# Kernel optimization log

Measured on AMD Instinct MI355X. Metric: run time of the kernel, lower is better.

## Reference

```python
import jax, jax.numpy as jnp
import numpy as np

B, T, D = 4096, 200, 64
H = 32  # hidden units of score MLP
NEG_INF = jnp.float32(-2**32 + 1)


def setup_inputs() -> dict:
    key = jax.random.key(0)
    k1, k2, k3, k4, k5 = jax.random.split(key, 5)
    query = jax.random.normal(k1, (B, 1, D), dtype=jnp.float32)
    keys = jax.random.normal(k2, (B, T, D), dtype=jnp.float32)
    mask = jax.random.randint(k3, (B, T), 0, 2) > 0
    mask = mask.at[:, 0].set(True)  # ensure at least one valid key per row
    # Glorot-normal-ish init for the tiny score MLP
    W1 = jax.random.normal(k4, (3 * D, H), dtype=jnp.float32) * jnp.sqrt(2.0 / (3 * D + H))
    b1 = jnp.zeros((H,), dtype=jnp.float32)
    W2 = jax.random.normal(k5, (H, 1), dtype=jnp.float32) * jnp.sqrt(2.0 / (H + 1))
    b2 = jnp.zeros((1,), dtype=jnp.float32)
    return {"query": query, "keys": keys, "mask": mask,
            "W1": W1, "b1": b1, "W2": W2, "b2": b2}


def reference(query, keys, mask, W1, b1, W2, b2):
    b, t, d = keys.shape
    q = jnp.broadcast_to(query, (b, t, d))            # tile query over seq
    att_in = jnp.concatenate([q, keys, q - keys], axis=-1)   # [B,T,3D]
    h = jax.nn.sigmoid(att_in @ W1 + b1)              # [B,T,H]
    score = (h @ W2 + b2)[..., 0]                     # [B,T]
    score = jnp.where(mask, score, NEG_INF)
    w = jax.nn.softmax(score, axis=-1)                # [B,T]
    out = jnp.einsum('bt,btd->bd', w, keys)           # weighted key sum
    return out[:, None, :]                            # [B,1,D]
```

## Files before the change

### kernel.cpp

```cpp
#include <hip/hip_runtime.h>
#include <hip/hip_bf16.h>


#define B 4096
#define T 200
#define D 64
#define H 32
#define LOG2E 1.44269504088896340736f
#define SOFF 16.0f
#define NTILE 13
#define PITCH 68

typedef __attribute__((ext_vector_type(8))) short short8;
typedef __attribute__((ext_vector_type(4))) float f32x4;


__global__ __launch_bounds__(256) void prep_kernel(
        const float* __restrict__ W1,
        const float* __restrict__ b1,
        const float* __restrict__ query,
        float*       __restrict__ ws)
{
    int blk = blockIdx.x;
    int tid = threadIdx.x;
    if (blk < 512) {
        int n = blk * 256 + tid;
        int b = n >> 5;
        int j = n & 31;
        const float* qb = query + (size_t)b * D;
        float acc = b1[j];
        #pragma unroll 8
        for (int i = 0; i < D; ++i)
            acc = fmaf(qb[i], W1[i * H + j] + W1[(128 + i) * H + j], acc);
        ws[n] = acc;
    } else if (blk < 520) {
        int m = (blk - 512) * 256 + tid;
        int e  = m & 7;
        int l  = (m >> 3) & 63;
        int fs = m >> 9;
        int ntile = fs >> 1, kstep = fs & 1;
        int k = kstep * 32 + (l >> 4) * 8 + e;
        int j = ntile * 16 + (l & 15);
        float v = W1[(64 + k) * H + j] - W1[(128 + k) * H + j];
        __hip_bfloat16 hv = __float2bfloat16(v);
        reinterpret_cast<unsigned short*>(ws + 131072)[m] =
            __builtin_bit_cast(unsigned short, hv);
    } else {
        int z = (blk - 520) * 256 + tid;
        float4 zz = {0.f, 0.f, 0.f, 0.f};
        reinterpret_cast<float4*>(ws + 132096)[z] = zz;
    }
}

__device__ __forceinline__ unsigned short bf16u(float x) {
    __hip_bfloat16 h = __float2bfloat16(x);
    return __builtin_bit_cast(unsigned short, h);
}

__global__ __launch_bounds__(256) void attn_pool_kernel(
        const float* __restrict__ keys,
        const int*   __restrict__ mask,
        const unsigned short* __restrict__ wkf,
        const float* __restrict__ qa_all,
        const float* __restrict__ W2,
        float*       __restrict__ num,
        float*       __restrict__ den)
{
    __shared__ float wkbuf[4][16 * PITCH];

    const int tid  = threadIdx.x;
    const int wv   = tid >> 6;
    const int lane = tid & 63;
    const int quad = lane >> 4;
    const int l15  = lane & 15;

    const int gid  = blockIdx.x * 4 + wv;
    const int b    = (int)(((unsigned)gid * 20165u) >> 18);
    const int tile = gid - b * NTILE;

    const short8* wf = reinterpret_cast<const short8*>(wkf);
    short8 bf0 = wf[0 * 64 + lane];
    short8 bf1 = wf[1 * 64 + lane];
    short8 bf2 = wf[2 * 64 + lane];
    short8 bf3 = wf[3 * 64 + lane];

    const float* qa = qa_all + (size_t)b * H;
    const float qa0 = qa[l15];
    const float qa1 = qa[16 + l15];
    const float w20 = W2[l15];
    const float w21 = W2[16 + l15];

    const int t  = tile * 16 + l15;
    const int tr = (t < T) ? t : (T - 1);

    const float4* krow = reinterpret_cast<const float4*>(keys + (size_t)b * (T * D));
    float4 k0 = krow[tr * 16 + quad * 2 + 0];
    float4 k1 = krow[tr * 16 + quad * 2 + 1];
    float4 k2 = krow[tr * 16 + 8 + quad * 2 + 0];
    float4 k3 = krow[tr * 16 + 8 + quad * 2 + 1];
    const int mval = mask[(size_t)b * T + tr];

    short8 a0, a1;
    a0[0] = (short)bf16u(k0.x); a0[1] = (short)bf16u(k0.y);
    a0[2] = (short)bf16u(k0.z); a0[3] = (short)bf16u(k0.w);
    a0[4] = (short)bf16u(k1.x); a0[5] = (short)bf16u(k1.y);
    a0[6] = (short)bf16u(k1.z); a0[7] = (short)bf16u(k1.w);
    a1[0] = (short)bf16u(k2.x); a1[1] = (short)bf16u(k2.y);
    a1[2] = (short)bf16u(k2.z); a1[3] = (short)bf16u(k2.w);
    a1[4] = (short)bf16u(k3.x); a1[5] = (short)bf16u(k3.y);
    a1[6] = (short)bf16u(k3.z); a1[7] = (short)bf16u(k3.w);

    f32x4 c0 = {0.f, 0.f, 0.f, 0.f};
    f32x4 c1 = {0.f, 0.f, 0.f, 0.f};
    c0 = __builtin_amdgcn_mfma_f32_16x16x32_bf16(a0, bf0, c0, 0, 0, 0);
    c0 = __builtin_amdgcn_mfma_f32_16x16x32_bf16(a1, bf1, c0, 0, 0, 0);
    c1 = __builtin_amdgcn_mfma_f32_16x16x32_bf16(a0, bf2, c1, 0, 0, 0);
    c1 = __builtin_amdgcn_mfma_f32_16x16x32_bf16(a1, bf3, c1, 0, 0, 0);

    float p[4];
    #pragma unroll
    for (int r = 0; r < 4; ++r) {
        float x0 = c0[r] + qa0;
        float x1 = c1[r] + qa1;
        float s0 = __builtin_amdgcn_rcpf(1.0f + exp2f(-x0 * LOG2E));
        float s1 = __builtin_amdgcn_rcpf(1.0f + exp2f(-x1 * LOG2E));
        p[r] = fmaf(s0, w20, s1 * w21);
    }
    #pragma unroll
    for (int r = 0; r < 4; ++r) {
        #pragma unroll
        for (int off = 1; off <= 8; off <<= 1)
            p[r] += __shfl_xor(p[r], off, 64);
    }
    const int addr = (l15 >> 2) << 6;
    int q0 = __builtin_amdgcn_ds_bpermute(addr, __builtin_bit_cast(int, p[0]));
    int q1 = __builtin_amdgcn_ds_bpermute(addr, __builtin_bit_cast(int, p[1]));
    int q2 = __builtin_amdgcn_ds_bpermute(addr, __builtin_bit_cast(int, p[2]));
    int q3 = __builtin_amdgcn_ds_bpermute(addr, __builtin_bit_cast(int, p[3]));
    const int rsel = l15 & 3;
    int s01 = (rsel & 1) ? q1 : q0;
    int s23 = (rsel & 1) ? q3 : q2;
    float st = __builtin_bit_cast(float, (rsel & 2) ? s23 : s01);

    const float w = ((t < T) && (mval != 0)) ? exp2f((st - SOFF) * LOG2E) : 0.0f;

    float* wb = wkbuf[wv];
    float4 wk0 = {w * k0.x, w * k0.y, w * k0.z, w * k0.w};
    float4 wk1 = {w * k1.x, w * k1.y, w * k1.z, w * k1.w};
    float4 wk2 = {w * k2.x, w * k2.y, w * k2.z, w * k2.w};
    float4 wk3 = {w * k3.x, w * k3.y, w * k3.z, w * k3.w};
    *reinterpret_cast<float4*>(&wb[l15 * PITCH + quad * 8 + 0]) = wk0;
    *reinterpret_cast<float4*>(&wb[l15 * PITCH + quad * 8 + 4]) = wk1;
    *reinterpret_cast<float4*>(&wb[l15 * PITCH + 32 + quad * 8 + 0]) = wk2;
    *reinterpret_cast<float4*>(&wb[l15 * PITCH + 32 + quad * 8 + 4]) = wk3;

    float dw = w;
    #pragma unroll
    for (int off = 1; off <= 8; off <<= 1)
        dw += __shfl_xor(dw, off, 64);

    float colsum = 0.0f;
    #pragma unroll
    for (int tt = 0; tt < 16; ++tt)
        colsum += wb[tt * PITCH + lane];

    atomicAdd(&num[(size_t)b * D + lane], colsum);
    if (lane == 0) atomicAdd(&den[b], dw);
}

__global__ __launch_bounds__(256) void finalize_kernel(
        const float* __restrict__ num, const float* __restrict__ den,
        float* __restrict__ out)
{
    int i = blockIdx.x * 256 + threadIdx.x;
    out[i] = num[i] * __builtin_amdgcn_rcpf(den[i >> 6]);
}

extern "C" void kernel_launch(void* const* d_in, const int* in_sizes, int n_in,
                              void* d_out, int out_size, void* d_ws, size_t ws_size,
                              hipStream_t stream) {
    const float* query = (const float*)d_in[0];
    const float* keys  = (const float*)d_in[1];
    const int*   mask  = (const int*)d_in[2];
    const float* W1    = (const float*)d_in[3];
    const float* b1    = (const float*)d_in[4];
    const float* W2    = (const float*)d_in[5];

    float* ws = (float*)d_ws;
    float* qa = ws;
    unsigned short* wkf = (unsigned short*)(ws + 131072);
    float* num = ws + 132096;
    float* den = ws + 132096 + 262144;

    prep_kernel<<<780, 256, 0, stream>>>(W1, b1, query, ws);
    attn_pool_kernel<<<(B * NTILE) / 4, 256, 0, stream>>>(keys, mask, wkf, qa, W2,
                                                          num, den);
    finalize_kernel<<<(B * D) / 256, 256, 0, stream>>>(num, den, (float*)d_out);
}
```

Before: 303.4 us.

## Process a full batch row per wavefront and drop atomics and finalize kernel

Each wavefront now loops over all 13 time tiles of one batch row and keeps the weighted key sums and denominator in registers, prefetching the next tile's keys while computing the current one. This removes the zero-init pass, the LDS staging buffer, the global atomics on num/den and the separate finalize launch, and writes normalized outputs directly. In exchange the grid shrinks from ~13k blocks to 1024 blocks, so there is less parallelism for hiding memory latency, and it adds a 16-register accumulator with cross-lane shuffle reductions.

```diff
diff --git a/kernel.cpp b/kernel.cpp
--- a/kernel.cpp
+++ b/kernel.cpp
@@ -9,7 +9,6 @@
 #define LOG2E 1.44269504088896340736f
 #define SOFF 16.0f
 #define NTILE 13
-#define PITCH 68
 
 typedef __attribute__((ext_vector_type(8))) short short8;
 typedef __attribute__((ext_vector_type(4))) float f32x4;
@@ -33,7 +32,7 @@
         for (int i = 0; i < D; ++i)
             acc = fmaf(qb[i], W1[i * H + j] + W1[(128 + i) * H + j], acc);
         ws[n] = acc;
-    } else if (blk < 520) {
+    } else {
         int m = (blk - 512) * 256 + tid;
         int e  = m & 7;
         int l  = (m >> 3) & 63;
@@ -45,10 +44,6 @@
         __hip_bfloat16 hv = __float2bfloat16(v);
         reinterpret_cast<unsigned short*>(ws + 131072)[m] =
             __builtin_bit_cast(unsigned short, hv);
-    } else {
-        int z = (blk - 520) * 256 + tid;
-        float4 zz = {0.f, 0.f, 0.f, 0.f};
-        reinterpret_cast<float4*>(ws + 132096)[z] = zz;
     }
 }
 
@@ -57,26 +52,21 @@
     return __builtin_bit_cast(unsigned short, h);
 }
 
-__global__ __launch_bounds__(256) void attn_pool_kernel(
+__global__ __launch_bounds__(256, 4) void attn_pool_kernel(
         const float* __restrict__ keys,
         const int*   __restrict__ mask,
         const unsigned short* __restrict__ wkf,
         const float* __restrict__ qa_all,
         const float* __restrict__ W2,
-        float*       __restrict__ num,
-        float*       __restrict__ den)
+        float*       __restrict__ out)
 {
-    __shared__ float wkbuf[4][16 * PITCH];
-
     const int tid  = threadIdx.x;
     const int wv   = tid >> 6;
     const int lane = tid & 63;
     const int quad = lane >> 4;
     const int l15  = lane & 15;
 
-    const int gid  = blockIdx.x * 4 + wv;
-    const int b    = (int)(((unsigned)gid * 20165u) >> 18);
-    const int tile = gid - b * NTILE;
+    const int b = blockIdx.x * 4 + wv;
 
     const short8* wf = reinterpret_cast<const short8*>(wkf);
     short8 bf0 = wf[0 * 64 + lane];
@@ -90,90 +80,115 @@
     const float w20 = W2[l15];
     const float w21 = W2[16 + l15];
 
-    const int t  = tile * 16 + l15;
-    const int tr = (t < T) ? t : (T - 1);
-
     const float4* krow = reinterpret_cast<const float4*>(keys + (size_t)b * (T * D));
-    float4 k0 = krow[tr * 16 + quad * 2 + 0];
-    float4 k1 = krow[tr * 16 + quad * 2 + 1];
-    float4 k2 = krow[tr * 16 + 8 + quad * 2 + 0];
-    float4 k3 = krow[tr * 16 + 8 + quad * 2 + 1];
-    const int mval = mask[(size_t)b * T + tr];
-
-    short8 a0, a1;
-    a0[0] = (short)bf16u(k0.x); a0[1] = (short)bf16u(k0.y);
-    a0[2] = (short)bf16u(k0.z); a0[3] = (short)bf16u(k0.w);
-    a0[4] = (short)bf16u(k1.x); a0[5] = (short)bf16u(k1.y);
-    a0[6] = (short)bf16u(k1.z); a0[7] = (short)bf16u(k1.w);
-    a1[0] = (short)bf16u(k2.x); a1[1] = (short)bf16u(k2.y);
-    a1[2] = (short)bf16u(k2.z); a1[3] = (short)bf16u(k2.w);
-    a1[4] = (short)bf16u(k3.x); a1[5] = (short)bf16u(k3.y);
-    a1[6] = (short)bf16u(k3.z); a1[7] = (short)bf16u(k3.w);
-
-    f32x4 c0 = {0.f, 0.f, 0.f, 0.f};
-    f32x4 c1 = {0.f, 0.f, 0.f, 0.f};
-    c0 = __builtin_amdgcn_mfma_f32_16x16x32_bf16(a0, bf0, c0, 0, 0, 0);
-    c0 = __builtin_amdgcn_mfma_f32_16x16x32_bf16(a1, bf1, c0, 0, 0, 0);
-    c1 = __builtin_amdgcn_mfma_f32_16x16x32_bf16(a0, bf2, c1, 0, 0, 0);
-    c1 = __builtin_amdgcn_mfma_f32_16x16x32_bf16(a1, bf3, c1, 0, 0, 0);
-
-    float p[4];
-    #pragma unroll
-    for (int r = 0; r < 4; ++r) {
-        float x0 = c0[r] + qa0;
-        float x1 = c1[r] + qa1;
-        float s0 = __builtin_amdgcn_rcpf(1.0f + exp2f(-x0 * LOG2E));
-        float s1 = __builtin_amdgcn_rcpf(1.0f + exp2f(-x1 * LOG2E));
-        p[r] = fmaf(s0, w20, s1 * w21);
-    }
-    #pragma unroll
-    for (int r = 0; r < 4; ++r) {
+    const int*    mrow = mask + (size_t)b * T;
+    const int ib = quad * 2;
+
+    float acc[16];
+    #pragma unroll
+    for (int j = 0; j < 16; ++j) acc[j] = 0.0f;
+    float dacc = 0.0f;
+
+    float4 kA0 = krow[l15 * 16 + ib + 0];
+    float4 kA1 = krow[l15 * 16 + ib + 1];
+    float4 kA2 = krow[l15 * 16 + 8 + ib + 0];
+    float4 kA3 = krow[l15 * 16 + 8 + ib + 1];
+    int    mA  = mrow[l15];
+
+    #pragma unroll
+    for (int tile = 0; tile < NTILE; ++tile) {
+        float4 kB0 = kA0, kB1 = kA1, kB2 = kA2, kB3 = kA3;
+        int    mB  = mA;
+        if (tile + 1 < NTILE) {
+            int tn  = (tile + 1) * 16 + l15;
+            int trn = (tn < T) ? tn : (T - 1);
+            kB0 = krow[trn * 16 + ib + 0];
+            kB1 = krow[trn * 16 + ib + 1];
+            kB2 = krow[trn * 16 + 8 + ib + 0];
+            kB3 = krow[trn * 16 + 8 + ib + 1];
+            mB  = mrow[trn];
+        }
+
+        short8 a0, a1;
+        a0[0] = (short)bf16u(kA0.x); a0[1] = (short)bf16u(kA0.y);
+        a0[2] = (short)bf16u(kA0.z); a0[3] = (short)bf16u(kA0.w);
+        a0[4] = (short)bf16u(kA1.x); a0[5] = (short)bf16u(kA1.y);
+        a0[6] = (short)bf16u(kA1.z); a0[7] = (short)bf16u(kA1.w);
+        a1[0] = (short)bf16u(kA2.x); a1[1] = (short)bf16u(kA2.y);
+        a1[2] = (short)bf16u(kA2.z); a1[3] = (short)bf16u(kA2.w);
+        a1[4] = (short)bf16u(kA3.x); a1[5] = (short)bf16u(kA3.y);
+        a1[6] = (short)bf16u(kA3.z); a1[7] = (short)bf16u(kA3.w);
+
+        f32x4 c0 = {0.f, 0.f, 0.f, 0.f};
+        f32x4 c1 = {0.f, 0.f, 0.f, 0.f};
+        c0 = __builtin_amdgcn_mfma_f32_16x16x32_bf16(a0, bf0, c0, 0, 0, 0);
+        c0 = __builtin_amdgcn_mfma_f32_16x16x32_bf16(a1, bf1, c0, 0, 0, 0);
+        c1 = __builtin_amdgcn_mfma_f32_16x16x32_bf16(a0, bf2, c1, 0, 0, 0);
+        c1 = __builtin_amdgcn_mfma_f32_16x16x32_bf16(a1, bf3, c1, 0, 0, 0);
+
+        float p[4];
+        #pragma unroll
+        for (int r = 0; r < 4; ++r) {
+            float x0 = c0[r] + qa0;
+            float x1 = c1[r] + qa1;
+            float s0 = __builtin_amdgcn_rcpf(1.0f + exp2f(-x0 * LOG2E));
+            float s1 = __builtin_amdgcn_rcpf(1.0f + exp2f(-x1 * LOG2E));
+            p[r] = fmaf(s0, w20, s1 * w21);
+        }
+        #pragma unroll
+        for (int r = 0; r < 4; ++r) {
+            #pragma unroll
+            for (int off = 1; off <= 8; off <<= 1)
+                p[r] += __shfl_xor(p[r], off, 64);
+        }
+        const int addr = (l15 >> 2) << 6;
+        int q0 = __builtin_amdgcn_ds_bpermute(addr, __builtin_bit_cast(int, p[0]));
+        int q1 = __builtin_amdgcn_ds_bpermute(addr, __builtin_bit_cast(int, p[1]));
+        int q2 = __builtin_amdgcn_ds_bpermute(addr, __builtin_bit_cast(int, p[2]));
+        int q3 = __builtin_amdgcn_ds_bpermute(addr, __builtin_bit_cast(int, p[3]));
+        const int rsel = l15 & 3;
+        int s01 = (rsel & 1) ? q1 : q0;
+        int s23 = (rsel & 1) ? q3 : q2;
+        float st = __builtin_bit_cast(float, (rsel & 2) ? s23 : s01);
+
+        const int t = tile * 16 + l15;
+        const float w = ((t < T) && (mA != 0)) ? exp2f((st - SOFF) * LOG2E) : 0.0f;
+
+        acc[0]  = fmaf(w, kA0.x, acc[0]);  acc[1]  = fmaf(w, kA0.y, acc[1]);
+        acc[2]  = fmaf(w, kA0.z, acc[2]);  acc[3]  = fmaf(w, kA0.w, acc[3]);
+        acc[4]  = fmaf(w, kA1.x, acc[4]);  acc[5]  = fmaf(w, kA1.y, acc[5]);
+        acc[6]  = fmaf(w, kA1.z, acc[6]);  acc[7]  = fmaf(w, kA1.w, acc[7]);
+        acc[8]  = fmaf(w, kA2.x, acc[8]);  acc[9]  = fmaf(w, kA2.y, acc[9]);
+        acc[10] = fmaf(w, kA2.z, acc[10]); acc[11] = fmaf(w, kA2.w, acc[11]);
+        acc[12] = fmaf(w, kA3.x, acc[12]); acc[13] = fmaf(w, kA3.y, acc[13]);
+        acc[14] = fmaf(w, kA3.z, acc[14]); acc[15] = fmaf(w, kA3.w, acc[15]);
+        dacc += w;
+
+        kA0 = kB0; kA1 = kB1; kA2 = kB2; kA3 = kB3; mA = mB;
+    }
+
+    #pragma unroll
+    for (int j = 0; j < 16; ++j) {
         #pragma unroll
         for (int off = 1; off <= 8; off <<= 1)
-            p[r] += __shfl_xor(p[r], off, 64);
-    }
-    const int addr = (l15 >> 2) << 6;
-    int q0 = __builtin_amdgcn_ds_bpermute(addr, __builtin_bit_cast(int, p[0]));
-    int q1 = __builtin_amdgcn_ds_bpermute(addr, __builtin_bit_cast(int, p[1]));
-    int q2 = __builtin_amdgcn_ds_bpermute(addr, __builtin_bit_cast(int, p[2]));
-    int q3 = __builtin_amdgcn_ds_bpermute(addr, __builtin_bit_cast(int, p[3]));
-    const int rsel = l15 & 3;
-    int s01 = (rsel & 1) ? q1 : q0;
-    int s23 = (rsel & 1) ? q3 : q2;
-    float st = __builtin_bit_cast(float, (rsel & 2) ? s23 : s01);
-
-    const float w = ((t < T) && (mval != 0)) ? exp2f((st - SOFF) * LOG2E) : 0.0f;
-
-    float* wb = wkbuf[wv];
-    float4 wk0 = {w * k0.x, w * k0.y, w * k0.z, w * k0.w};
-    float4 wk1 = {w * k1.x, w * k1.y, w * k1.z, w * k1.w};
-    float4 wk2 = {w * k2.x, w * k2.y, w * k2.z, w * k2.w};
-    float4 wk3 = {w * k3.x, w * k3.y, w * k3.z, w * k3.w};
-    *reinterpret_cast<float4*>(&wb[l15 * PITCH + quad * 8 + 0]) = wk0;
-    *reinterpret_cast<float4*>(&wb[l15 * PITCH + quad * 8 + 4]) = wk1;
-    *reinterpret_cast<float4*>(&wb[l15 * PITCH + 32 + quad * 8 + 0]) = wk2;
-    *reinterpret_cast<float4*>(&wb[l15 * PITCH + 32 + quad * 8 + 4]) = wk3;
-
-    float dw = w;
+            acc[j] += __shfl_xor(acc[j], off, 64);
+    }
     #pragma unroll
     for (int off = 1; off <= 8; off <<= 1)
-        dw += __shfl_xor(dw, off, 64);
-
-    float colsum = 0.0f;
-    #pragma unroll
-    for (int tt = 0; tt < 16; ++tt)
-        colsum += wb[tt * PITCH + lane];
-
-    atomicAdd(&num[(size_t)b * D + lane], colsum);
-    if (lane == 0) atomicAdd(&den[b], dw);
-}
-
-__global__ __launch_bounds__(256) void finalize_kernel(
-        const float* __restrict__ num, const float* __restrict__ den,
-        float* __restrict__ out)
-{
-    int i = blockIdx.x * 256 + threadIdx.x;
-    out[i] = num[i] * __builtin_amdgcn_rcpf(den[i >> 6]);
+        dacc += __shfl_xor(dacc, off, 64);
+
+    if (l15 == 0) {
+        float rw = __builtin_amdgcn_rcpf(dacc);
+        float4 o0 = {acc[0]  * rw, acc[1]  * rw, acc[2]  * rw, acc[3]  * rw};
+        float4 o1 = {acc[4]  * rw, acc[5]  * rw, acc[6]  * rw, acc[7]  * rw};
+        float4 o2 = {acc[8]  * rw, acc[9]  * rw, acc[10] * rw, acc[11] * rw};
+        float4 o3 = {acc[12] * rw, acc[13] * rw, acc[14] * rw, acc[15] * rw};
+        float4* ob = reinterpret_cast<float4*>(out + (size_t)b * D);
+        ob[ib + 0]     = o0;
+        ob[ib + 1]     = o1;
+        ob[8 + ib + 0] = o2;
+        ob[8 + ib + 1] = o3;
+    }
 }
 
 extern "C" void kernel_launch(void* const* d_in, const int* in_sizes, int n_in,
@@ -189,11 +204,8 @@
     float* ws = (float*)d_ws;
     float* qa = ws;
     unsigned short* wkf = (unsigned short*)(ws + 131072);
-    float* num = ws + 132096;
-    float* den = ws + 132096 + 262144;
-
-    prep_kernel<<<780, 256, 0, stream>>>(W1, b1, query, ws);
-    attn_pool_kernel<<<(B * NTILE) / 4, 256, 0, stream>>>(keys, mask, wkf, qa, W2,
-                                                          num, den);
-    finalize_kernel<<<(B * D) / 256, 256, 0, stream>>>(num, den, (float*)d_out);
-}
+
+    prep_kernel<<<520, 256, 0, stream>>>(W1, b1, query, ws);
+    attn_pool_kernel<<<B / 4, 256, 0, stream>>>(keys, mask, wkf, qa, W2,
+                                                (float*)d_out);
+}
```

Result: slower. 365.3 us (+20.4%).
